# Kernel optimization log

Hardware: AMD Instinct MI355X
Metric: run time of the kernel (lower is better)

The kernel has to match this reference:

```python
import jax, jax.numpy as jnp
import numpy as np

TGT, BSZ, E = 256, 8, 256
SRC = 4096
H = 8
HD = E // H


def setup_inputs() -> dict:
    key = jax.random.key(0)
    ks = jax.random.split(key, 6)
    return {
        "query": jax.random.normal(ks[0], (TGT, BSZ, E), dtype=jnp.float32),
        "key": jax.random.normal(ks[1], (SRC, BSZ, E), dtype=jnp.float32),
        "value": jax.random.normal(ks[2], (SRC, BSZ, E), dtype=jnp.float32),
        "proposal_mask": jax.random.uniform(ks[3], (BSZ, TGT, SRC), dtype=jnp.float32),
        "out_proj_weight": jax.random.normal(ks[4], (E, E), dtype=jnp.float32) * (1.0 / np.sqrt(E)),
        "out_proj_bias": jax.random.normal(ks[5], (E,), dtype=jnp.float32) * 0.01,
    }


def reference(query, key, value, proposal_mask, out_proj_weight, out_proj_bias):
    tgt_len, bsz, embed_dim = query.shape
    src_len = key.shape[0]
    num_heads = H
    head_dim = embed_dim // num_heads

    # v: (src, bsz, E) -> (src, bsz*H, hd) -> (bsz*H, src, hd); index q = b*H + h
    v = value.reshape(src_len, bsz * num_heads, head_dim).transpose(1, 0, 2)

    # proposal_mask (bsz, tgt, src); torch loop+stack produces mask_nhead[b*H+h] = proposal_mask[b]
    mask_nhead = jnp.repeat(proposal_mask, num_heads, axis=0)  # (bsz*H, tgt, src)

    # weighted sum of values per head (no score compute)
    attn_output = jnp.einsum('qts,qsc->qtc', mask_nhead, v)  # (bsz*H, tgt, hd)

    # (bsz*H, tgt, hd) -> (tgt, bsz*H, hd) -> (tgt, bsz, E)
    attn_output = attn_output.transpose(1, 0, 2).reshape(tgt_len, bsz, embed_dim)

    # out projection (outDecoderLayer=False)
    attn_output = attn_output @ out_proj_weight.T + out_proj_bias

    # averaged weights: mask repeated per head -> mean over heads == proposal_mask
    attn_weights = mask_nhead.reshape(bsz, num_heads, tgt_len, src_len).sum(axis=1) / num_heads
    return attn_output, attn_weights
```

## Files before the change

### kernel.cpp

```cpp
#include <hip/hip_runtime.h>
#include <hip/hip_bf16.h>

#define TGT 256
#define BSZ 8
#define E   256
#define SRC 4096

typedef __attribute__((ext_vector_type(8))) short           bf16x8;
typedef __attribute__((ext_vector_type(4))) float           f32x4;
typedef __attribute__((ext_vector_type(4))) float           f4;
typedef __attribute__((ext_vector_type(8))) unsigned short  u16x8;

__device__ inline unsigned short f2b(float x) {
    union { __hip_bfloat16 h; unsigned short u; } cv;
    cv.h = __float2bfloat16(x);
    return cv.u;
}

__device__ inline bf16x8 cvt8v(const float* __restrict__ p) {
    f4 lo = *(const f4*)p;
    f4 hi = *(const f4*)(p + 4);
    bf16x8 r;
    #pragma unroll
    for (int j = 0; j < 4; ++j) { r[j] = (short)f2b(lo[j]); r[4 + j] = (short)f2b(hi[j]); }
    return r;
}

__global__ __launch_bounds__(256) void prep(
    const float* __restrict__ value, const float* __restrict__ wgt,
    unsigned short* __restrict__ vtf, unsigned short* __restrict__ wf)
{
    const int tid = threadIdx.x;

    if (blockIdx.y == 8) {
        if (tid < 128) {
            int o    = blockIdx.x * 128 + tid;
            int et   = o >> 9;
            int ks   = (o >> 6) & 7;
            int lane = o & 63;
            int quad = lane >> 4, l15 = lane & 15;
            bf16x8 v = cvt8v(wgt + (size_t)(et * 16 + l15) * E + ks * 32 + quad * 8);
            *(bf16x8*)&wf[(size_t)o * 8] = v;
        }
        return;
    }

    __shared__ unsigned short tile[64 * 264];
    const int kch = blockIdx.x;
    const int b   = blockIdx.y;
    const int k0  = kch * 64;

    #pragma unroll
    for (int i = 0; i < 16; ++i) {
        int lin = i * 256 + tid;
        int row = lin >> 6;
        int c4  = lin & 63;
        f4 v = *(const f4*)(value + (size_t)(k0 + row) * (BSZ * E)
                                  + (size_t)b * E + c4 * 4);
        #pragma unroll
        for (int j = 0; j < 4; ++j) tile[row * 264 + c4 * 4 + j] = f2b(v[j]);
    }
    __syncthreads();

    #pragma unroll
    for (int i = 0; i < 8; ++i) {
        int o    = i * 256 + tid;
        int et   = o >> 7;
        int ksl  = (o >> 6) & 1;
        int lane = o & 63;
        int quad = lane >> 4, l15 = lane & 15;
        u16x8 pk;
        #pragma unroll
        for (int j = 0; j < 8; ++j)
            pk[j] = tile[(ksl * 32 + quad * 8 + j) * 264 + et * 16 + l15];
        size_t ks = (size_t)kch * 2 + ksl;
        *(u16x8*)&vtf[((((size_t)b * 16 + et) * 128 + ks) * 64 + lane) * 8] = pk;
    }
}

#define AP 136

__global__ __launch_bounds__(512) void gemm1(
    const float* __restrict__ mask,
    const unsigned short* __restrict__ vtf,
    float* __restrict__ out1,
    float* __restrict__ part)
{
    __shared__ unsigned short As[2][32 * AP];
    const int bx  = blockIdx.x;
    const int b   = bx & 7;
    const int tt  = (bx >> 3) & 7;
    const int kc  = bx >> 6;
    const int t0  = tt * 32;
    const int k0  = kc * 512;
    const int tid = threadIdx.x;
    const int w    = tid >> 6;
    const int lane = tid & 63;
    const int quad = lane >> 4;
    const int l15  = lane & 15;

    const float* mbase = mask + (size_t)b * TGT * SRC + (size_t)t0 * SRC + k0;
    float*       obase = out1 + (size_t)b * TGT * SRC + (size_t)t0 * SRC + k0;
    const int sr0 = tid >> 5, sr1 = sr0 + 16, sc = (tid & 31) * 4;

    const unsigned short* bfr0 = vtf + (((size_t)b * 16 + 2 * w) * 128 + (size_t)kc * 16) * 512;
    const unsigned short* bfr1 = bfr0 + (size_t)128 * 512;

    {
        f4 v0 = *(const f4*)(mbase + (size_t)sr0 * SRC + sc);
        f4 v1 = *(const f4*)(mbase + (size_t)sr1 * SRC + sc);
        *(f4*)(obase + (size_t)sr0 * SRC + sc) = v0;
        *(f4*)(obase + (size_t)sr1 * SRC + sc) = v1;
        unsigned short* d0 = &As[0][sr0 * AP + sc];
        unsigned short* d1 = &As[0][sr1 * AP + sc];
        #pragma unroll
        for (int j = 0; j < 4; ++j) { d0[j] = f2b(v0[j]); d1[j] = f2b(v1[j]); }
    }
    __syncthreads();

    f32x4 acc00 = {}, acc01 = {}, acc10 = {}, acc11 = {};

    #pragma unroll
    for (int s = 0; s < 4; ++s) {
        f4 a0v, a1v;
        if (s < 3) {
            a0v = *(const f4*)(mbase + (size_t)sr0 * SRC + (s + 1) * 128 + sc);
            a1v = *(const f4*)(mbase + (size_t)sr1 * SRC + (s + 1) * 128 + sc);
        }
        #pragma unroll
        for (int q = 0; q < 4; ++q) {
            bf16x8 B0 = *(const bf16x8*)(bfr0 + ((size_t)(s * 4 + q) * 64 + lane) * 8);
            bf16x8 B1 = *(const bf16x8*)(bfr1 + ((size_t)(s * 4 + q) * 64 + lane) * 8);
            bf16x8 a0 = *(const bf16x8*)&As[s & 1][ l15       * AP + q * 32 + quad * 8];
            bf16x8 a1 = *(const bf16x8*)&As[s & 1][(l15 + 16) * AP + q * 32 + quad * 8];
            acc00 = __builtin_amdgcn_mfma_f32_16x16x32_bf16(a0, B0, acc00, 0, 0, 0);
            acc01 = __builtin_amdgcn_mfma_f32_16x16x32_bf16(a0, B1, acc01, 0, 0, 0);
            acc10 = __builtin_amdgcn_mfma_f32_16x16x32_bf16(a1, B0, acc10, 0, 0, 0);
            acc11 = __builtin_amdgcn_mfma_f32_16x16x32_bf16(a1, B1, acc11, 0, 0, 0);
        }
        if (s < 3) {
            *(f4*)(obase + (size_t)sr0 * SRC + (s + 1) * 128 + sc) = a0v;
            *(f4*)(obase + (size_t)sr1 * SRC + (s + 1) * 128 + sc) = a1v;
            unsigned short* d0 = &As[(s + 1) & 1][sr0 * AP + sc];
            unsigned short* d1 = &As[(s + 1) & 1][sr1 * AP + sc];
            #pragma unroll
            for (int j = 0; j < 4; ++j) { d0[j] = f2b(a0v[j]); d1[j] = f2b(a1v[j]); }
        }
        __syncthreads();
    }

    float* pb = part + ((size_t)kc * BSZ + b) * TGT * E;
    #pragma unroll
    for (int r = 0; r < 4; ++r) {
        int rr0 = t0 + quad * 4 + r;
        int rr1 = rr0 + 16;
        int c0  = w * 32 + l15;
        pb[(size_t)rr0 * E + c0]      = acc00[r];
        pb[(size_t)rr0 * E + c0 + 16] = acc01[r];
        pb[(size_t)rr1 * E + c0]      = acc10[r];
        pb[(size_t)rr1 * E + c0 + 16] = acc11[r];
    }
}

#define PSTRIDE ((size_t)BSZ * TGT * E)

__global__ __launch_bounds__(256) void gemm2_fused(
    const float* __restrict__ part,
    const unsigned short* __restrict__ wf,
    const float* __restrict__ bias,
    float* __restrict__ out0)
{
    __shared__ unsigned short ct[16 * 264];
    const int blk  = blockIdx.x;
    const int b    = blk & 7;
    const int tt16 = blk >> 3;
    const int tid  = threadIdx.x;

    const float* pb = part + (size_t)b * TGT * E + (size_t)(tt16 * 16) * E;
    #pragma unroll
    for (int i = 0; i < 4; ++i) {
        int idx = i * 256 + tid;
        int row = idx >> 6;
        int c4  = idx & 63;
        const float* ap = pb + (size_t)row * E + c4 * 4;
        f4 s = *(const f4*)ap;
        #pragma unroll
        for (int p = 1; p < 8; ++p) s += *(const f4*)(ap + p * PSTRIDE);
        #pragma unroll
        for (int j = 0; j < 4; ++j) ct[row * 264 + c4 * 4 + j] = f2b(s[j]);
    }
    __syncthreads();

    const int w    = tid >> 6;
    const int lane = tid & 63;
    const int quad = lane >> 4;
    const int l15  = lane & 15;

    bf16x8 A[8];
    #pragma unroll
    for (int ks = 0; ks < 8; ++ks)
        A[ks] = *(const bf16x8*)&ct[l15 * 264 + ks * 32 + quad * 8];

    #pragma unroll
    for (int e4 = 0; e4 < 4; ++e4) {
        int et = w * 4 + e4;
        const unsigned short* bf = wf + ((size_t)et * 8 * 64 + lane) * 8;
        f32x4 acc = {};
        #pragma unroll
        for (int ks = 0; ks < 8; ++ks) {
            bf16x8 bb = *(const bf16x8*)(bf + (size_t)ks * 512);
            acc = __builtin_amdgcn_mfma_f32_16x16x32_bf16(A[ks], bb, acc, 0, 0, 0);
        }
        const float bval = bias[et * 16 + l15];
        #pragma unroll
        for (int r = 0; r < 4; ++r) {
            int t = tt16 * 16 + quad * 4 + r;
            int e = et * 16 + l15;
            out0[(size_t)t * (BSZ * E) + (size_t)b * E + e] = acc[r] + bval;
        }
    }
}

extern "C" void kernel_launch(void* const* d_in, const int* in_sizes, int n_in,
                              void* d_out, int out_size, void* d_ws, size_t ws_size,
                              hipStream_t stream)
{
    const float* value = (const float*)d_in[2];
    const float* mask  = (const float*)d_in[3];
    const float* wgt   = (const float*)d_in[4];
    const float* bias  = (const float*)d_in[5];

    float* out0 = (float*)d_out;
    float* out1 = (float*)d_out + (size_t)TGT * BSZ * E;

    unsigned short* vtf  = (unsigned short*)d_ws;
    unsigned short* wf   = vtf + (size_t)BSZ * E * SRC;
    float*          part = (float*)(wf + (size_t)16 * 8 * 64 * 8);

    prep<<<dim3(64, 9), 256, 0, stream>>>(value, wgt, vtf, wf);
    gemm1<<<512, 512, 0, stream>>>(mask, vtf, out1, part);
    gemm2_fused<<<128, 256, 0, stream>>>(part, wf, bias, out0);
}
```

Baseline: 150.0 us.

## Fuse output projection into gemm1 epilogue with atomic accumulation, drop split-K partials

Each gemm1 block now converts its split-K partial attention tile to bf16 in shared memory, multiplies it by the projection weight, and atomically adds the result into the output. The prep kernel pre-fills the output with the bias. This removes the fp32 partial buffer round trip and the third kernel launch. In exchange it issues many fp32 atomics (8 split-K contributions per output element) and rounds each partial to bf16 before the projection, which changes numerics slightly and makes summation order nondeterministic.

```diff
diff --git a/kernel.cpp b/kernel.cpp
--- a/kernel.cpp
+++ b/kernel.cpp
@@ -28,9 +28,20 @@
 
 __global__ __launch_bounds__(256) void prep(
     const float* __restrict__ value, const float* __restrict__ wgt,
-    unsigned short* __restrict__ vtf, unsigned short* __restrict__ wf)
+    const float* __restrict__ bias,
+    unsigned short* __restrict__ vtf, unsigned short* __restrict__ wf,
+    float* __restrict__ out0)
 {
     const int tid = threadIdx.x;
+
+    if (blockIdx.y == 9) {
+        #pragma unroll
+        for (int s = 0; s < 8; ++s) {
+            int f4i = s * 16384 + blockIdx.x * 256 + tid;
+            *(f4*)(out0 + (size_t)f4i * 4) = *(const f4*)(bias + (f4i & 63) * 4);
+        }
+        return;
+    }
 
     if (blockIdx.y == 8) {
         if (tid < 128) {
@@ -79,12 +90,14 @@
 }
 
 #define AP 136
+#define CP 264
 
 __global__ __launch_bounds__(512) void gemm1(
     const float* __restrict__ mask,
     const unsigned short* __restrict__ vtf,
+    const unsigned short* __restrict__ wf,
     float* __restrict__ out1,
-    float* __restrict__ part)
+    float* __restrict__ out0)
 {
     __shared__ unsigned short As[2][32 * AP];
     const int bx  = blockIdx.x;
@@ -149,74 +162,47 @@
         __syncthreads();
     }
 
-    float* pb = part + ((size_t)kc * BSZ + b) * TGT * E;
-    #pragma unroll
-    for (int r = 0; r < 4; ++r) {
-        int rr0 = t0 + quad * 4 + r;
-        int rr1 = rr0 + 16;
-        int c0  = w * 32 + l15;
-        pb[(size_t)rr0 * E + c0]      = acc00[r];
-        pb[(size_t)rr0 * E + c0 + 16] = acc01[r];
-        pb[(size_t)rr1 * E + c0]      = acc10[r];
-        pb[(size_t)rr1 * E + c0 + 16] = acc11[r];
-    }
-}
-
-#define PSTRIDE ((size_t)BSZ * TGT * E)
-
-__global__ __launch_bounds__(256) void gemm2_fused(
-    const float* __restrict__ part,
-    const unsigned short* __restrict__ wf,
-    const float* __restrict__ bias,
-    float* __restrict__ out0)
-{
-    __shared__ unsigned short ct[16 * 264];
-    const int blk  = blockIdx.x;
-    const int b    = blk & 7;
-    const int tt16 = blk >> 3;
-    const int tid  = threadIdx.x;
-
-    const float* pb = part + (size_t)b * TGT * E + (size_t)(tt16 * 16) * E;
-    #pragma unroll
-    for (int i = 0; i < 4; ++i) {
-        int idx = i * 256 + tid;
-        int row = idx >> 6;
-        int c4  = idx & 63;
-        const float* ap = pb + (size_t)row * E + c4 * 4;
-        f4 s = *(const f4*)ap;
-        #pragma unroll
-        for (int p = 1; p < 8; ++p) s += *(const f4*)(ap + p * PSTRIDE);
-        #pragma unroll
-        for (int j = 0; j < 4; ++j) ct[row * 264 + c4 * 4 + j] = f2b(s[j]);
+    unsigned short* ct = &As[0][0];
+    {
+        const int c0 = w * 32 + l15;
+        #pragma unroll
+        for (int r = 0; r < 4; ++r) {
+            int r0 = quad * 4 + r;
+            ct[ r0       * CP + c0     ] = f2b(acc00[r]);
+            ct[ r0       * CP + c0 + 16] = f2b(acc01[r]);
+            ct[(r0 + 16) * CP + c0     ] = f2b(acc10[r]);
+            ct[(r0 + 16) * CP + c0 + 16] = f2b(acc11[r]);
+        }
     }
     __syncthreads();
 
-    const int w    = tid >> 6;
-    const int lane = tid & 63;
-    const int quad = lane >> 4;
-    const int l15  = lane & 15;
-
-    bf16x8 A[8];
-    #pragma unroll
-    for (int ks = 0; ks < 8; ++ks)
-        A[ks] = *(const bf16x8*)&ct[l15 * 264 + ks * 32 + quad * 8];
-
-    #pragma unroll
-    for (int e4 = 0; e4 < 4; ++e4) {
-        int et = w * 4 + e4;
-        const unsigned short* bf = wf + ((size_t)et * 8 * 64 + lane) * 8;
-        f32x4 acc = {};
+    {
+        const int et0 = 2 * w;
+        const unsigned short* bf0 = wf + ((size_t)et0 * 8 * 64 + lane) * 8;
+        const unsigned short* bf1 = bf0 + (size_t)8 * 64 * 8;
+        f32x4 p00 = {}, p01 = {}, p10 = {}, p11 = {};
         #pragma unroll
         for (int ks = 0; ks < 8; ++ks) {
-            bf16x8 bb = *(const bf16x8*)(bf + (size_t)ks * 512);
-            acc = __builtin_amdgcn_mfma_f32_16x16x32_bf16(A[ks], bb, acc, 0, 0, 0);
-        }
-        const float bval = bias[et * 16 + l15];
+            bf16x8 aLo = *(const bf16x8*)&ct[ l15       * CP + ks * 32 + quad * 8];
+            bf16x8 aHi = *(const bf16x8*)&ct[(l15 + 16) * CP + ks * 32 + quad * 8];
+            bf16x8 b0  = *(const bf16x8*)(bf0 + (size_t)ks * 512);
+            bf16x8 b1  = *(const bf16x8*)(bf1 + (size_t)ks * 512);
+            p00 = __builtin_amdgcn_mfma_f32_16x16x32_bf16(aLo, b0, p00, 0, 0, 0);
+            p01 = __builtin_amdgcn_mfma_f32_16x16x32_bf16(aLo, b1, p01, 0, 0, 0);
+            p10 = __builtin_amdgcn_mfma_f32_16x16x32_bf16(aHi, b0, p10, 0, 0, 0);
+            p11 = __builtin_amdgcn_mfma_f32_16x16x32_bf16(aHi, b1, p11, 0, 0, 0);
+        }
         #pragma unroll
         for (int r = 0; r < 4; ++r) {
-            int t = tt16 * 16 + quad * 4 + r;
-            int e = et * 16 + l15;
-            out0[(size_t)t * (BSZ * E) + (size_t)b * E + e] = acc[r] + bval;
+            int tA = t0 + quad * 4 + r;
+            int tB = tA + 16;
+            int eA = et0 * 16 + l15;
+            float* oA = out0 + (size_t)tA * (BSZ * E) + (size_t)b * E;
+            float* oB = out0 + (size_t)tB * (BSZ * E) + (size_t)b * E;
+            atomicAdd(oA + eA,      p00[r]);
+            atomicAdd(oA + eA + 16, p01[r]);
+            atomicAdd(oB + eA,      p10[r]);
+            atomicAdd(oB + eA + 16, p11[r]);
         }
     }
 }
@@ -235,9 +221,7 @@
 
     unsigned short* vtf  = (unsigned short*)d_ws;
     unsigned short* wf   = vtf + (size_t)BSZ * E * SRC;
-    float*          part = (float*)(wf + (size_t)16 * 8 * 64 * 8);
-
-    prep<<<dim3(64, 9), 256, 0, stream>>>(value, wgt, vtf, wf);
-    gemm1<<<512, 512, 0, stream>>>(mask, vtf, out1, part);
-    gemm2_fused<<<128, 256, 0, stream>>>(part, wf, bias, out0);
-}
+
+    prep<<<dim3(64, 10), 256, 0, stream>>>(value, wgt, bias, vtf, wf, out0);
+    gemm1<<<512, 512, 0, stream>>>(mask, vtf, wf, out1, out0);
+}
```

Result: no change. 150.4 us (+0.2%).
